# Kernel optimization log

Measured on AMD Instinct MI355X. Metric: run time of the kernel, lower is better.

Reference implementation:

```python
import jax, jax.numpy as jnp
import numpy as np
from math import sqrt

B, NQ, SK, ISIZE, HSIZE, OSIZE, H = 4, 2048, 2048, 1024, 1024, 1024, 16
D = HSIZE // H  # attn_dim = 64
IEPS = 1e-32
NEG = -1e32

def setup_inputs() -> dict:
    key = jax.random.key(0)
    ks = jax.random.split(key, 9)
    scale = 1.0 / sqrt(ISIZE)
    return {
        "iQ": jax.random.normal(ks[0], (B, NQ, ISIZE), jnp.float32),
        "iK": jax.random.normal(ks[1], (B, SK, ISIZE), jnp.float32),
        "iV": jax.random.normal(ks[2], (B, SK, ISIZE), jnp.float32),
        "mask": jax.random.randint(ks[3], (B, NQ, SK), 0, 2).astype(bool),
        # torch nn.Linear weights: [out_features, in_features]
        "Wq": jax.random.normal(ks[4], (HSIZE, ISIZE), jnp.float32) * scale,
        "Wk": jax.random.normal(ks[5], (HSIZE, ISIZE), jnp.float32) * scale,
        "Wv": jax.random.normal(ks[6], (HSIZE, ISIZE), jnp.float32) * scale,
        "Wo": jax.random.normal(ks[7], (OSIZE, HSIZE), jnp.float32) * scale,
        "sn_bias": jnp.zeros((1,), jnp.float32),  # SparseNormer bias
    }

def reference(iQ, iK, iV, mask, Wq, Wk, Wv, Wo, sn_bias):
    b, nq, _ = iQ.shape
    sk = iK.shape[1]
    # projections, split into heads: [b, h, n, d]
    q = (iQ @ Wq.T).reshape(b, nq, H, D).transpose(0, 2, 1, 3)
    k = (iK @ Wk.T).reshape(b, sk, H, D).transpose(0, 2, 1, 3)
    v = (iV @ Wv.T).reshape(b, sk, H, D).transpose(0, 2, 1, 3)
    # scaled dot-product scores: [b, h, nq, sk]
    scores = jnp.einsum("bhqd,bhkd->bhqk", q, k) / sqrt(D)
    scores = jnp.where(mask[:, None, :, :], NEG, scores)
    # SparseNormer: relu(x + bias)^2 normalized along last dim
    t = jax.nn.relu(scores + sn_bias)
    t = t * t
    attn = t / (t.sum(-1, keepdims=True) + IEPS)
    o = jnp.einsum("bhqk,bhkd->bhqd", attn, v)
    o = o.transpose(0, 2, 1, 3).reshape(b, nq, HSIZE)
    return o @ Wo.T
```

## Files before the change

kernel.cpp:

```cpp
#include <hip/hip_runtime.h>
#include <stdint.h>

#define B_   4
#define NQ_  2048
#define SK_  2048
#define H_   16
#define HS_  1024
#define D_   64
#define TOKc ((size_t)B_ * NQ_ * HS_)
#define WEc  ((size_t)HS_ * HS_)

typedef __attribute__((ext_vector_type(8))) short bf16x8;
typedef __attribute__((ext_vector_type(4))) float f32x4;
typedef __attribute__((ext_vector_type(2))) float f32x2;
typedef __attribute__((ext_vector_type(8))) unsigned short u16x8;
typedef __attribute__((ext_vector_type(4))) int i32x4;

#define DEVI __device__ __forceinline__

DEVI unsigned short f2bf_hu(float f) {
  union { float f; unsigned int i; } x; x.f = f;
  return (unsigned short)((x.i + 0x8000u) >> 16);
}
DEVI unsigned int pack2(float a, float b) {
  union { float f; unsigned int i; } x, y; x.f = a; y.f = b;
  return __builtin_amdgcn_perm(y.i + 0x8000u, x.i + 0x8000u, 0x07060302u);
}
DEVI u16x8 cvt8(f32x4 lo, f32x4 hi) {
  union { u16x8 s; unsigned int w[4]; } r;
  r.w[0] = pack2(lo[0], lo[1]);
  r.w[1] = pack2(lo[2], lo[3]);
  r.w[2] = pack2(hi[0], hi[1]);
  r.w[3] = pack2(hi[2], hi[3]);
  return r.s;
}
DEVI void async16(void* lds, const void* g) {
  __builtin_amdgcn_global_load_lds(
      (const __attribute__((address_space(1))) unsigned int*)g,
      (__attribute__((address_space(3))) unsigned int*)lds, 16, 0, 0);
}

DEVI f32x2 pkfma(f32x2 a, f32x2 b, f32x2 c) {
  f32x2 d;
  asm("v_pk_fma_f32 %0, %1, %2, %3" : "=v"(d) : "v"(a), "v"(b), "v"(c));
  return d;
}
DEVI f32x2 pkmul(f32x2 a, f32x2 b) {
  f32x2 d;
  asm("v_pk_mul_f32 %0, %1, %2" : "=v"(d) : "v"(a), "v"(b));
  return d;
}
DEVI f32x2 pkadd(f32x2 a, f32x2 b) {
  f32x2 d;
  asm("v_pk_add_f32 %0, %1, %2" : "=v"(d) : "v"(a), "v"(b));
  return d;
}
DEVI unsigned int cvtpk_bf16(float lo, float hi) {
  unsigned int r;
  asm("v_cvt_pk_bf16_f32 %0, %1, %2" : "=v"(r) : "v"(lo), "v"(hi));
  return r;
}
template <int OFF>
DEVI float keepf(float x, unsigned int nb) {
  int k;
  asm("v_bfe_i32 %0, %1, %2, 1" : "=v"(k) : "v"(nb), "i"(OFF));
  union { float f; int i; } u; u.f = x; u.i &= k;
  return u.f;
}

#define SWZB(row, colb) ((((row) * 128) + (colb)) ^ (((row) & 7) << 4))

__global__ __launch_bounds__(256)
void cvt_prep(const float* __restrict__ a, unsigned short* __restrict__ ab,
              const float* __restrict__ wsrc, unsigned short* __restrict__ wdst,
              int naBlocks) {
  const int bi = blockIdx.x;
  const float* s; unsigned short* d; size_t base;
  if (bi < naBlocks) { s = a;    d = ab;   base = (size_t)bi * 2048; }
  else               { s = wsrc; d = wdst; base = (size_t)(bi - naBlocks) * 2048; }
  const size_t o = base + (size_t)threadIdx.x * 8;
  f32x4 lo = *(const f32x4*)(s + o);
  f32x4 hi = *(const f32x4*)(s + o + 4);
  *(u16x8*)(d + o) = cvt8(lo, hi);
}

__global__ __launch_bounds__(256)
void cvt_all(const float* __restrict__ iQ, const float* __restrict__ iK,
             const float* __restrict__ iV, const float* __restrict__ Wq,
             const float* __restrict__ Wk, const float* __restrict__ Wv,
             const float* __restrict__ Wo, unsigned short* __restrict__ ACT,
             unsigned short* __restrict__ WALL) {
  const int bi = blockIdx.x;
  const float* s; unsigned short* d; size_t base;
  if (bi < 12288) {
    const int which = bi >> 12;
    s = (which == 0) ? iQ : (which == 1) ? iK : iV;
    d = ACT + (size_t)which * TOKc;
    base = (size_t)(bi & 4095) * 2048;
  } else {
    const int wi = (bi - 12288) >> 9;
    s = (wi == 0) ? Wq : (wi == 1) ? Wk : (wi == 2) ? Wv : Wo;
    d = WALL + (size_t)wi * WEc;
    base = (size_t)((bi - 12288) & 511) * 2048;
  }
  const size_t o = base + (size_t)threadIdx.x * 8;
  f32x4 lo = *(const f32x4*)(s + o);
  f32x4 hi = *(const f32x4*)(s + o + 4);
  *(u16x8*)(d + o) = cvt8(lo, hi);
}

__global__ __launch_bounds__(256)
void pack_mask(const int* __restrict__ m, unsigned long long* __restrict__ bits) {
  const size_t tid = (size_t)blockIdx.x * 256 + threadIdx.x;
  const unsigned long long bal = __ballot(m[tid] != 0);
  if ((threadIdx.x & 63) == 0) bits[tid >> 6] = bal;
}

template <bool CF32>
DEVI void gemm_body(const unsigned short* __restrict__ A,
                    const unsigned short* __restrict__ Wb,
                    void* __restrict__ Cp, int M, int N, int K,
                    unsigned short* As, unsigned short* Bs) {
  const int t = threadIdx.x;
  const int w = t >> 6, l = t & 63;
  const int lm = l & 15, lg = l >> 4;
  const int bm = blockIdx.x * 128, bn = blockIdx.y * 128;
  const int wm = (w >> 1) * 64, wn = (w & 1) * 64;

  const int sr = t >> 2;
  const int sg = ((t & 3) ^ ((t >> 3) & 3)) * 8;
  const unsigned short* Ag0 = A + (size_t)(bm + sr) * K + sg;
  const unsigned short* Ag1 = A + (size_t)(bm + sr + 64) * K + sg;
  const unsigned short* Wg0 = Wb + (size_t)(bn + sr) * K + sg;
  const unsigned short* Wg1 = Wb + (size_t)(bn + sr + 64) * K + sg;
  unsigned short* lA0 = &As[t * 8];
  unsigned short* lA1 = &As[t * 8 + 2048];
  unsigned short* lB0 = &Bs[t * 8];
  unsigned short* lB1 = &Bs[t * 8 + 2048];

  const int fx = (lm >> 1) & 3;
  f32x4 acc[4][4] = {};

  for (int k0 = 0; k0 < K; k0 += 32) {
    async16(lA0, Ag0 + k0);
    async16(lA1, Ag1 + k0);
    async16(lB0, Wg0 + k0);
    async16(lB1, Wg1 + k0);
    __syncthreads();
    bf16x8 aF[4], bF[4];
#pragma unroll
    for (int i = 0; i < 4; i++)
      aF[i] = *(const bf16x8*)&As[(wm + i * 16 + lm) * 32 + ((lg ^ fx) * 8)];
#pragma unroll
    for (int i = 0; i < 4; i++)
      bF[i] = *(const bf16x8*)&Bs[(wn + i * 16 + lm) * 32 + ((lg ^ fx) * 8)];
    __builtin_amdgcn_s_setprio(1);
#pragma unroll
    for (int i = 0; i < 4; i++)
#pragma unroll
      for (int j = 0; j < 4; j++)
        acc[i][j] = __builtin_amdgcn_mfma_f32_16x16x32_bf16(aF[i], bF[j], acc[i][j], 0, 0, 0);
    __builtin_amdgcn_s_setprio(0);
    __syncthreads();
  }
#pragma unroll
  for (int i = 0; i < 4; i++)
#pragma unroll
    for (int j = 0; j < 4; j++) {
      const int row = bm + wm + i * 16 + lg * 4;
      const int col = bn + wn + j * 16 + lm;
#pragma unroll
      for (int r = 0; r < 4; r++) {
        if constexpr (CF32) {
          ((float*)Cp)[(size_t)(row + r) * N + col] = acc[i][j][r];
        } else {
          ((unsigned short*)Cp)[(size_t)(row + r) * N + col] = f2bf_hu(acc[i][j][r]);
        }
      }
    }
}

template <bool CF32>
__global__ __launch_bounds__(256)
void gemm_bb(const unsigned short* __restrict__ A, const unsigned short* __restrict__ Wb,
             void* __restrict__ Cp, int M, int N, int K) {
  __shared__ unsigned short As[128 * 32];
  __shared__ unsigned short Bs[128 * 32];
  gemm_body<CF32>(A, Wb, Cp, M, N, K, As, Bs);
}

__global__ __launch_bounds__(256)
void gemm_qkv(const unsigned short* __restrict__ ACT, const unsigned short* __restrict__ WALL,
              unsigned short* __restrict__ Qb, unsigned short* __restrict__ Kb,
              unsigned short* __restrict__ Vb, int M, int N, int K) {
  __shared__ unsigned short As[128 * 32];
  __shared__ unsigned short Bs[128 * 32];
  const int z = blockIdx.z;
  const unsigned short* A = ACT + (size_t)z * (size_t)M * (size_t)K;
  const unsigned short* W = WALL + (size_t)z * (size_t)N * (size_t)K;
  unsigned short* C = (z == 0) ? Qb : ((z == 1) ? Kb : Vb);
  gemm_body<false>(A, W, (void*)C, M, N, K, As, Bs);
}

template <bool ABF16, bool CF32>
__global__ __launch_bounds__(256)
void gemm_bt(const void* __restrict__ Ap, const float* __restrict__ W,
             void* __restrict__ Cp, int M, int N, int K) {
  __shared__ unsigned short As[128 * 40];
  __shared__ unsigned short Bs[128 * 40];
  const int t = threadIdx.x;
  const int w = t >> 6, l = t & 63;
  const int lm = l & 15, lg = l >> 4;
  const int bm = blockIdx.x * 128, bn = blockIdx.y * 128;
  const int wm = (w >> 1) * 64, wn = (w & 1) * 64;
  const int sr = t >> 2, sc = (t & 3) * 8;
  const float* Af = (const float*)Ap;
  const unsigned short* Ab = (const unsigned short*)Ap;
  const size_t ao0 = (size_t)(bm + sr) * K + sc;
  const size_t ao1 = (size_t)(bm + sr + 64) * K + sc;
  const size_t wo0 = (size_t)(bn + sr) * K + sc;
  const size_t wo1 = (size_t)(bn + sr + 64) * K + sc;
  auto loadA = [&](size_t off) -> u16x8 {
    if constexpr (ABF16) {
      return *(const u16x8*)(Ab + off);
    } else {
      f32x4 lo = *(const f32x4*)(Af + off);
      f32x4 hi = *(const f32x4*)(Af + off + 4);
      return cvt8(lo, hi);
    }
  };
  auto loadW = [&](size_t off) -> u16x8 {
    f32x4 lo = *(const f32x4*)(W + off);
    f32x4 hi = *(const f32x4*)(W + off + 4);
    return cvt8(lo, hi);
  };
  u16x8 pa0 = loadA(ao0), pa1 = loadA(ao1);
  u16x8 pb0 = loadW(wo0), pb1 = loadW(wo1);
  f32x4 acc[4][4] = {};
  for (int k0 = 0; k0 < K; k0 += 32) {
    *(u16x8*)&As[sr * 40 + sc]        = pa0;
    *(u16x8*)&As[(sr + 64) * 40 + sc] = pa1;
    *(u16x8*)&Bs[sr * 40 + sc]        = pb0;
    *(u16x8*)&Bs[(sr + 64) * 40 + sc] = pb1;
    __syncthreads();
    if (k0 + 32 < K) {
      pa0 = loadA(ao0 + k0 + 32);
      pa1 = loadA(ao1 + k0 + 32);
      pb0 = loadW(wo0 + k0 + 32);
      pb1 = loadW(wo1 + k0 + 32);
    }
    bf16x8 aF[4], bF[4];
#pragma unroll
    for (int i = 0; i < 4; i++)
      aF[i] = *(const bf16x8*)&As[(wm + i * 16 + lm) * 40 + lg * 8];
#pragma unroll
    for (int i = 0; i < 4; i++)
      bF[i] = *(const bf16x8*)&Bs[(wn + i * 16 + lm) * 40 + lg * 8];
#pragma unroll
    for (int i = 0; i < 4; i++)
#pragma unroll
      for (int j = 0; j < 4; j++)
        acc[i][j] = __builtin_amdgcn_mfma_f32_16x16x32_bf16(aF[i], bF[j], acc[i][j], 0, 0, 0);
    __syncthreads();
  }
#pragma unroll
  for (int i = 0; i < 4; i++)
#pragma unroll
    for (int j = 0; j < 4; j++) {
      const int row = bm + wm + i * 16 + lg * 4;
      const int col = bn + wn + j * 16 + lm;
#pragma unroll
      for (int r = 0; r < 4; r++) {
        if constexpr (CF32) {
          ((float*)Cp)[(size_t)(row + r) * N + col] = acc[i][j][r];
        } else {
          ((unsigned short*)Cp)[(size_t)(row + r) * N + col] = f2bf_hu(acc[i][j][r]);
        }
      }
    }
}

template <int MODE>
__global__ __launch_bounds__(256)
void attn_sn(const unsigned short* __restrict__ Qb,
             const unsigned short* __restrict__ Kb,
             const unsigned short* __restrict__ Vb,
             const int* __restrict__ mask,
             const unsigned int* __restrict__ bits,
             const float* __restrict__ snb,
             unsigned short* __restrict__ Ob) {
  __shared__ unsigned short Ks[64 * 64];
  __shared__ unsigned short Vt[64 * 64];
  __shared__ unsigned short Pq[128 * 64];

  const int h = blockIdx.x, qt = blockIdx.y, b = blockIdx.z;
  const int t = threadIdx.x, w = t >> 6, l = t & 63;
  const int lm = l & 15, lg = l >> 4;
  const int q0 = qt * 128;
  const int wk = (w >> 1) * 32;
  const int wn = (w & 1) * 64;
  const float bias = snb[0];

  char* KsB = (char*)Ks;
  char* VtB = (char*)Vt;
  char* PqB = (char*)Pq;

  bf16x8 bQ[4][2];
#pragma unroll
  for (int ni = 0; ni < 4; ni++)
#pragma unroll
    for (int kf = 0; kf < 2; kf++) {
      const int qq = q0 + wn + ni * 16 + lm;
      bQ[ni][kf] = *(const bf16x8*)&Qb[(size_t)(b * NQ_ + qq) * HS_ + h * D_ + kf * 32 + lg * 8];
    }

  const int kr = t >> 3, kcb = (t & 7) * 16;
  const unsigned short* Kg = Kb + (size_t)(b * SK_) * HS_ + h * D_ + (t & 7) * 8;
  const int va = t & 31;
  const int vc = (t >> 5) * 8;
  const unsigned short* Vg = Vb + (size_t)(b * SK_) * HS_ + h * D_ + vc;
  const int* mbase = mask + (size_t)b * NQ_ * SK_;

  f32x4 oacc[2][4] = {};
  float dpart[4] = {0.f, 0.f, 0.f, 0.f};
  f32x2 dp2[4] = {};

  u16x8 pk0 = *(const u16x8*)(Kg + (size_t)(kr) * HS_);
  u16x8 pk1 = *(const u16x8*)(Kg + (size_t)(32 + kr) * HS_);
  u16x8 pv0 = *(const u16x8*)(Vg + (size_t)(2 * va) * HS_);
  u16x8 pv1 = *(const u16x8*)(Vg + (size_t)(2 * va + 1) * HS_);

  for (int kt = 0; kt < SK_ / 64; kt++) {
    const int kk0 = kt * 64;
    *(u16x8*)(KsB + SWZB(kr, kcb))      = pk0;
    *(u16x8*)(KsB + SWZB(kr + 32, kcb)) = pk1;
    {
      union { u16x8 s; unsigned int w4[4]; } a0, a1;
      a0.s = pv0; a1.s = pv1;
#pragma unroll
      for (int ww = 0; ww < 4; ww++) {
        unsigned int lo = __builtin_amdgcn_perm(a1.w4[ww], a0.w4[ww], 0x05040100u);
        unsigned int hi = __builtin_amdgcn_perm(a1.w4[ww], a0.w4[ww], 0x07060302u);
        *(unsigned int*)(VtB + SWZB(vc + 2 * ww,     4 * va)) = lo;
        *(unsigned int*)(VtB + SWZB(vc + 2 * ww + 1, 4 * va)) = hi;
      }
    }
    __syncthreads();

    if (kt + 1 < SK_ / 64) {
      const int nk0 = kk0 + 64;
      pk0 = *(const u16x8*)(Kg + (size_t)(nk0 + kr) * HS_);
      pk1 = *(const u16x8*)(Kg + (size_t)(nk0 + 32 + kr) * HS_);
      pv0 = *(const u16x8*)(Vg + (size_t)(nk0 + 2 * va) * HS_);
      pv1 = *(const u16x8*)(Vg + (size_t)(nk0 + 2 * va + 1) * HS_);
    }

    i32x4 mq[4][2];
    unsigned int mb[4];
    if constexpr (MODE == 1) {
#pragma unroll
      for (int ni = 0; ni < 4; ni++)
        mb[ni] = bits[(size_t)(b * NQ_ + q0 + wn + ni * 16 + lm) * 64 + kt * 2 + (wk >> 5)];
    } else {
#pragma unroll
      for (int ni = 0; ni < 4; ni++) {
        const int* mrow = mbase + (size_t)(q0 + wn + ni * 16 + lm) * SK_ + kk0 + wk + lg * 4;
#pragma unroll
        for (int mi = 0; mi < 2; mi++) mq[ni][mi] = *(const i32x4*)(mrow + mi * 16);
      }
    }

    bf16x8 aK[2][2];
#pragma unroll
    for (int mi = 0; mi < 2; mi++)
#pragma unroll
      for (int kf = 0; kf < 2; kf++)
        aK[mi][kf] = *(const bf16x8*)(KsB + SWZB(wk + mi * 16 + lm, kf * 64 + lg * 16));
    f32x4 sf[2][4] = {};
    __builtin_amdgcn_s_setprio(1);
#pragma unroll
    for (int mi = 0; mi < 2; mi++)
#pragma unroll
      for (int ni = 0; ni < 4; ni++) {
        sf[mi][ni] = __builtin_amdgcn_mfma_f32_16x16x32_bf16(aK[mi][0], bQ[ni][0], sf[mi][ni], 0, 0, 0);
        sf[mi][ni] = __builtin_amdgcn_mfma_f32_16x16x32_bf16(aK[mi][1], bQ[ni][1], sf[mi][ni], 0, 0, 0);
      }
    __builtin_amdgcn_s_setprio(0);

    if constexpr (MODE == 1) {
      const f32x2 c8 = {0.125f, 0.125f};
      const f32x2 bias2 = {bias, bias};
#pragma unroll
      for (int ni = 0; ni < 4; ni++) {
        const unsigned int nb = (~mb[ni]) >> (lg * 4);
#pragma unroll
        for (int mi = 0; mi < 2; mi++) {
          const f32x4 sv = sf[mi][ni];
          f32x2 t01 = pkfma((f32x2){sv[0], sv[1]}, c8, bias2);
          f32x2 t23 = pkfma((f32x2){sv[2], sv[3]}, c8, bias2);
          float x0 = fmaxf(t01[0], 0.f), x1 = fmaxf(t01[1], 0.f);
          float x2 = fmaxf(t23[0], 0.f), x3 = fmaxf(t23[1], 0.f);
          if (mi == 0) {
            x0 = keepf<0>(x0, nb);  x1 = keepf<1>(x1, nb);
            x2 = keepf<2>(x2, nb);  x3 = keepf<3>(x3, nb);
          } else {
            x0 = keepf<16>(x0, nb); x1 = keepf<17>(x1, nb);
            x2 = keepf<18>(x2, nb); x3 = keepf<19>(x3, nb);
          }
          const f32x2 u01 = pkmul((f32x2){x0, x1}, (f32x2){x0, x1});
          const f32x2 u23 = pkmul((f32x2){x2, x3}, (f32x2){x2, x3});
          dp2[ni] = pkadd(dp2[ni], u01);
          dp2[ni] = pkadd(dp2[ni], u23);
          const unsigned long long pk =
              (unsigned long long)cvtpk_bf16(u01[0], u01[1]) |
              ((unsigned long long)cvtpk_bf16(u23[0], u23[1]) << 32);
          *(unsigned long long*)(PqB + SWZB(wn + ni * 16 + lm, (wk + mi * 16 + lg * 4) * 2)) = pk;
        }
      }
    } else {
#pragma unroll
      for (int ni = 0; ni < 4; ni++) {
        float dsum = 0.f;
#pragma unroll
        for (int mi = 0; mi < 2; mi++) {
          const f32x4 sv = sf[mi][ni];
          float x2[4];
#pragma unroll
          for (int r = 0; r < 4; r++) {
            float x = fmaxf(sv[r] * 0.125f + bias, 0.f);
            x = mq[ni][mi][r] ? 0.f : x;
            x2[r] = x * x;
            dsum += x2[r];
          }
          const unsigned long long pk =
              (unsigned long long)pack2(x2[0], x2[1]) |
              ((unsigned long long)pack2(x2[2], x2[3]) << 32);
          *(unsigned long long*)(PqB + SWZB(wn + ni * 16 + lm, (wk + mi * 16 + lg * 4) * 2)) = pk;
        }
        dpart[ni] += dsum;
      }
    }
    __syncthreads();

#pragma unroll
    for (int k2 = 0; k2 < 2; k2++) {
      bf16x8 aV[2], bP[4];
#pragma unroll
      for (int mi = 0; mi < 2; mi++)
        aV[mi] = *(const bf16x8*)(VtB + SWZB(wk + mi * 16 + lm, k2 * 64 + lg * 16));
#pragma unroll
      for (int ni = 0; ni < 4; ni++)
        bP[ni] = *(const bf16x8*)(PqB + SWZB(wn + ni * 16 + lm, k2 * 64 + lg * 16));
      __builtin_amdgcn_s_setprio(1);
#pragma unroll
      for (int mi = 0; mi < 2; mi++)
#pragma unroll
        for (int ni = 0; ni < 4; ni++)
          oacc[mi][ni] = __builtin_amdgcn_mfma_f32_16x16x32_bf16(aV[mi], bP[ni], oacc[mi][ni], 0, 0, 0);
      __builtin_amdgcn_s_setprio(0);
    }
    __syncthreads();
  }

  float* denomS = (float*)Ks;
#pragma unroll
  for (int ni = 0; ni < 4; ni++) {
    float v = (MODE == 1) ? (dp2[ni][0] + dp2[ni][1]) : dpart[ni];
    v += __shfl_xor(v, 16, 64);
    v += __shfl_xor(v, 32, 64);
    dpart[ni] = v;
  }
  if (((w >> 1) == 0) && (lg == 0)) {
#pragma unroll
    for (int ni = 0; ni < 4; ni++) denomS[wn + ni * 16 + lm] = dpart[ni];
  }
  __syncthreads();
  if (((w >> 1) == 1) && (lg == 0)) {
#pragma unroll
    for (int ni = 0; ni < 4; ni++) denomS[wn + ni * 16 + lm] += dpart[ni];
  }
  __syncthreads();

#pragma unroll
  for (int ni = 0; ni < 4; ni++) {
    const int ql = wn + ni * 16 + lm;
    const float inv = 1.0f / (denomS[ql] + 1e-32f);
#pragma unroll
    for (int mi = 0; mi < 2; mi++) {
      const int d0 = wk + mi * 16 + lg * 4;
      const f32x4 ov = oacc[mi][ni];
      const unsigned long long pk =
          (unsigned long long)cvtpk_bf16(ov[0] * inv, ov[1] * inv) |
          ((unsigned long long)cvtpk_bf16(ov[2] * inv, ov[3] * inv) << 32);
      *(unsigned long long*)(PqB + SWZB(ql, d0 * 2)) = pk;
    }
  }
  __syncthreads();
  const int qf = t >> 1;
  unsigned short* orow = Ob + (size_t)(b * NQ_ + q0 + qf) * HS_ + h * D_ + (t & 1) * 32;
#pragma unroll
  for (int j = 0; j < 4; j++) {
    u16x8 vv = *(const u16x8*)(PqB + SWZB(qf, (t & 1) * 64 + j * 16));
    *(u16x8*)(orow + j * 8) = vv;
  }
}

extern "C" void kernel_launch(void* const* d_in, const int* in_sizes, int n_in,
                              void* d_out, int out_size, void* d_ws, size_t ws_size,
                              hipStream_t stream) {
  (void)in_sizes; (void)n_in; (void)out_size;
  const float* iQ  = (const float*)d_in[0];
  const float* iK  = (const float*)d_in[1];
  const float* iV  = (const float*)d_in[2];
  const int*   msk = (const int*)d_in[3];
  const float* Wq  = (const float*)d_in[4];
  const float* Wk  = (const float*)d_in[5];
  const float* Wv  = (const float*)d_in[6];
  const float* Wo  = (const float*)d_in[7];
  const float* snb = (const float*)d_in[8];
  float* out = (float*)d_out;

  const size_t TOK = TOKc;
  const size_t WE  = WEc;
  const size_t BITS_B = (size_t)B_ * NQ_ * SK_ / 8;
  const size_t NEED1 = (3 * TOK + WE) * 2 + BITS_B;
  const size_t NEEDF = (6 * TOK + 4 * WE) * 2 + BITS_B;

  const dim3 gg(64, 8, 1), bb(256, 1, 1);
  const dim3 g3(64, 8, 3);
  const dim3 ga(H_, NQ_ / 128, B_);
  const int M = B_ * NQ_, N = HS_, K = HS_;

  if (ws_size >= NEEDF) {
    unsigned short* ACT  = (unsigned short*)d_ws;
    unsigned short* WALL = ACT + 3 * TOK;
    unsigned short* Kb   = WALL + 4 * WE;
    unsigned short* Vb   = Kb + TOK;
    unsigned short* Ob   = Vb + TOK;
    unsigned int*  bits  = (unsigned int*)(Ob + TOK);
    unsigned short* Qb   = (unsigned short*)d_out;
    unsigned short* Wob  = WALL + 3 * WE;

    hipLaunchKernelGGL(cvt_all, dim3(14336), bb, 0, stream,
                       iQ, iK, iV, Wq, Wk, Wv, Wo, ACT, WALL);
    hipLaunchKernelGGL(gemm_qkv, g3, bb, 0, stream, ACT, WALL, Qb, Kb, Vb, M, N, K);
    hipLaunchKernelGGL(pack_mask, dim3(65536), bb, 0, stream,
                       msk, (unsigned long long*)bits);
    hipLaunchKernelGGL((attn_sn<1>), ga, bb, 0, stream,
                       Qb, Kb, Vb, msk, bits, snb, Ob);
    hipLaunchKernelGGL((gemm_bb<true>), gg, bb, 0, stream, Ob, Wob, (void*)out, M, N, K);
  } else if (ws_size >= NEED1) {
    unsigned short* Kb = (unsigned short*)d_ws;
    unsigned short* Vb = Kb + TOK;
    unsigned short* Ob = Vb + TOK;
    unsigned short* Wb = Ob + TOK;
    unsigned int* bits = (unsigned int*)(Wb + WE);
    unsigned short* out_us = (unsigned short*)d_out;
    unsigned short* Qb  = out_us;
    unsigned short* INb = out_us + TOK;

    hipLaunchKernelGGL(cvt_prep, dim3(4608), bb, 0, stream, iQ, INb, Wq, Wb, 4096);
    hipLaunchKernelGGL((gemm_bb<false>), gg, bb, 0, stream, INb, Wb, (void*)Qb, M, N, K);
    hipLaunchKernelGGL(cvt_prep, dim3(4608), bb, 0, stream, iK, INb, Wk, Wb, 4096);
    hipLaunchKernelGGL((gemm_bb<false>), gg, bb, 0, stream, INb, Wb, (void*)Kb, M, N, K);
    hipLaunchKernelGGL(cvt_prep, dim3(4608), bb, 0, stream, iV, INb, Wv, Wb, 4096);
    hipLaunchKernelGGL((gemm_bb<false>), gg, bb, 0, stream, INb, Wb, (void*)Vb, M, N, K);
    hipLaunchKernelGGL(cvt_prep, dim3(512), bb, 0, stream,
                       (const float*)nullptr, (unsigned short*)nullptr, Wo, Wb, 0);
    hipLaunchKernelGGL(pack_mask, dim3(65536), bb, 0, stream,
                       msk, (unsigned long long*)bits);
    hipLaunchKernelGGL((attn_sn<1>), ga, bb, 0, stream,
                       Qb, Kb, Vb, msk, bits, snb, Ob);
    hipLaunchKernelGGL((gemm_bb<true>), gg, bb, 0, stream, Ob, Wb, (void*)out, M, N, K);
  } else {
    unsigned short *Qb, *Kb, *Vb, *Ob;
    if (ws_size >= 4 * TOK * sizeof(unsigned short)) {
      Qb = (unsigned short*)d_ws;
      Kb = Qb + TOK;
      Vb = Qb + 2 * TOK;
      Ob = Qb + 3 * TOK;
    } else {
      Qb = (unsigned short*)d_out;
      Kb = (unsigned short*)d_ws;
      Vb = Kb + TOK;
      Ob = Kb + 2 * TOK;
    }
    hipLaunchKernelGGL((gemm_bt<false, false>), gg, bb, 0, stream, (const void*)iQ, Wq, (void*)Qb, M, N, K);
    hipLaunchKernelGGL((gemm_bt<false, false>), gg, bb, 0, stream, (const void*)iK, Wk, (void*)Kb, M, N, K);
    hipLaunchKernelGGL((gemm_bt<false, false>), gg, bb, 0, stream, (const void*)iV, Wv, (void*)Vb, M, N, K);
    hipLaunchKernelGGL((attn_sn<0>), ga, bb, 0, stream,
                       Qb, Kb, Vb, msk, (const unsigned int*)nullptr, snb, Ob);
    hipLaunchKernelGGL((gemm_bt<true, true>), gg, bb, 0, stream, (const void*)Ob, Wo, (void*)out, M, N, K);
  }
}
```

Baseline: 441.8 us.

## Double-buffer LDS tiles in bf16 GEMM with async prefetch of next k-slice

Turns the bf16 GEMM body into a two-stage pipeline. Each iteration issues the async global-to-LDS loads for the next 32-wide k-slice into the other buffer before computing on the current one, and uses an explicit vmcnt wait plus raw barriers in place of the __syncthreads pairs. This aims to hide global load latency behind MFMA work in the QKV projection and output GEMMs, at the cost of twice the shared memory per block, which may lower occupancy.

```diff
diff --git a/kernel.cpp b/kernel.cpp
--- a/kernel.cpp
+++ b/kernel.cpp
@@ -117,10 +117,10 @@
 }
 
 template <bool CF32>
-DEVI void gemm_body(const unsigned short* __restrict__ A,
-                    const unsigned short* __restrict__ Wb,
-                    void* __restrict__ Cp, int M, int N, int K,
-                    unsigned short* As, unsigned short* Bs) {
+DEVI void gemm_body_pipe(const unsigned short* __restrict__ A,
+                         const unsigned short* __restrict__ Wb,
+                         void* __restrict__ Cp, int M, int N, int K,
+                         unsigned short* As, unsigned short* Bs) {
   const int t = threadIdx.x;
   const int w = t >> 6, l = t & 63;
   const int lm = l & 15, lg = l >> 4;
@@ -133,27 +133,39 @@
   const unsigned short* Ag1 = A + (size_t)(bm + sr + 64) * K + sg;
   const unsigned short* Wg0 = Wb + (size_t)(bn + sr) * K + sg;
   const unsigned short* Wg1 = Wb + (size_t)(bn + sr + 64) * K + sg;
-  unsigned short* lA0 = &As[t * 8];
-  unsigned short* lA1 = &As[t * 8 + 2048];
-  unsigned short* lB0 = &Bs[t * 8];
-  unsigned short* lB1 = &Bs[t * 8 + 2048];
 
   const int fx = (lm >> 1) & 3;
   f32x4 acc[4][4] = {};
 
+  auto stage = [&](int bi, int k0) {
+    unsigned short* la = As + bi * 4096 + t * 8;
+    unsigned short* lb = Bs + bi * 4096 + t * 8;
+    async16(la,        Ag0 + k0);
+    async16(la + 2048, Ag1 + k0);
+    async16(lb,        Wg0 + k0);
+    async16(lb + 2048, Wg1 + k0);
+  };
+
+  stage(0, 0);
+  int cur = 0;
   for (int k0 = 0; k0 < K; k0 += 32) {
-    async16(lA0, Ag0 + k0);
-    async16(lA1, Ag1 + k0);
-    async16(lB0, Wg0 + k0);
-    async16(lB1, Wg1 + k0);
-    __syncthreads();
+    if (k0 + 32 < K) {
+      stage(cur ^ 1, k0 + 32);
+      asm volatile("s_waitcnt vmcnt(4)" ::: "memory");
+    } else {
+      asm volatile("s_waitcnt vmcnt(0)" ::: "memory");
+    }
+    __builtin_amdgcn_sched_barrier(0);
+    __builtin_amdgcn_s_barrier();
+    const unsigned short* Ab = As + cur * 4096;
+    const unsigned short* Bb = Bs + cur * 4096;
     bf16x8 aF[4], bF[4];
 #pragma unroll
     for (int i = 0; i < 4; i++)
-      aF[i] = *(const bf16x8*)&As[(wm + i * 16 + lm) * 32 + ((lg ^ fx) * 8)];
+      aF[i] = *(const bf16x8*)&Ab[(wm + i * 16 + lm) * 32 + ((lg ^ fx) * 8)];
 #pragma unroll
     for (int i = 0; i < 4; i++)
-      bF[i] = *(const bf16x8*)&Bs[(wn + i * 16 + lm) * 32 + ((lg ^ fx) * 8)];
+      bF[i] = *(const bf16x8*)&Bb[(wn + i * 16 + lm) * 32 + ((lg ^ fx) * 8)];
     __builtin_amdgcn_s_setprio(1);
 #pragma unroll
     for (int i = 0; i < 4; i++)
@@ -161,7 +173,8 @@
       for (int j = 0; j < 4; j++)
         acc[i][j] = __builtin_amdgcn_mfma_f32_16x16x32_bf16(aF[i], bF[j], acc[i][j], 0, 0, 0);
     __builtin_amdgcn_s_setprio(0);
-    __syncthreads();
+    __builtin_amdgcn_s_barrier();
+    cur ^= 1;
   }
 #pragma unroll
   for (int i = 0; i < 4; i++)
@@ -184,22 +197,22 @@
 __global__ __launch_bounds__(256)
 void gemm_bb(const unsigned short* __restrict__ A, const unsigned short* __restrict__ Wb,
              void* __restrict__ Cp, int M, int N, int K) {
-  __shared__ unsigned short As[128 * 32];
-  __shared__ unsigned short Bs[128 * 32];
-  gemm_body<CF32>(A, Wb, Cp, M, N, K, As, Bs);
+  __shared__ unsigned short As[2 * 128 * 32];
+  __shared__ unsigned short Bs[2 * 128 * 32];
+  gemm_body_pipe<CF32>(A, Wb, Cp, M, N, K, As, Bs);
 }
 
 __global__ __launch_bounds__(256)
 void gemm_qkv(const unsigned short* __restrict__ ACT, const unsigned short* __restrict__ WALL,
               unsigned short* __restrict__ Qb, unsigned short* __restrict__ Kb,
               unsigned short* __restrict__ Vb, int M, int N, int K) {
-  __shared__ unsigned short As[128 * 32];
-  __shared__ unsigned short Bs[128 * 32];
+  __shared__ unsigned short As[2 * 128 * 32];
+  __shared__ unsigned short Bs[2 * 128 * 32];
   const int z = blockIdx.z;
   const unsigned short* A = ACT + (size_t)z * (size_t)M * (size_t)K;
   const unsigned short* W = WALL + (size_t)z * (size_t)N * (size_t)K;
   unsigned short* C = (z == 0) ? Qb : ((z == 1) ? Kb : Vb);
-  gemm_body<false>(A, W, (void*)C, M, N, K, As, Bs);
+  gemm_body_pipe<false>(A, W, (void*)C, M, N, K, As, Bs);
 }
 
 template <bool ABF16, bool CF32>
```

Result: no change. 443.6 us (+0.4%).
